# Performance work log

Hardware: AMD Instinct MI355X
Metric: run time of the kernel (lower is better)

The kernel has to match this reference:

```python
import math
import jax, jax.numpy as jnp
import numpy as np

D_MODEL = 1024
N_HEADS = 16
D_K = D_MODEL // N_HEADS


def _build_neighbours(n_heads):
    # Mirrors LatticeMultiHeadAttention._build_neighbours for a (4,4)-style lattice.
    side = int(math.sqrt(n_heads))
    cols = side + 1 if side * side < n_heads else side
    positions = [divmod(i, cols) for i in range(n_heads)]
    pos_map = {p: j for j, p in enumerate(positions)}
    nb_idx = np.full((n_heads, 8), -1, dtype=np.int64)
    nb_w = np.zeros((n_heads, 8), dtype=np.float32)
    for i, (r, c) in enumerate(positions):
        k = 0
        for dr in (-1, 0, 1):
            for dc in (-1, 0, 1):
                if dr == 0 and dc == 0:
                    continue
                j = pos_map.get((r + dr, c + dc))
                if j is not None and k < 8:
                    nb_idx[i, k] = j
                    nb_w[i, k] = math.exp(-math.hypot(dr, dc))
                    k += 1
    return nb_idx, nb_w


def _phase_biases(coupling):
    # Sequential Kuramoto phase update: head h uses neighbor phases already
    # updated for heads < h (exactly as the torch per-head loop mutates buffers).
    H = coupling.shape[0]
    nb_idx, nb_w = _build_neighbours(H)
    phases = [jnp.asarray(0.0, coupling.dtype) for _ in range(H)]
    two_pi = 2.0 * math.pi
    for h in range(H):
        force = jnp.asarray(0.0, coupling.dtype)
        for k in range(8):
            j = int(nb_idx[h, k])
            if j >= 0:
                force = force + jnp.asarray(nb_w[h, k], coupling.dtype) * jnp.sin(phases[j] - phases[h])
        intrinsic = 1.0 + 0.1 * h
        new_phase = (phases[h] + 0.01 * (intrinsic + coupling[h] * force)) % two_pi
        phases[h] = new_phase
    return 0.1 * jnp.cos(jnp.stack(phases))  # [H] per-head scalar bias


def setup_inputs() -> dict:
    key = jax.random.key(0)
    ks = jax.random.split(key, 9)
    B, L = 2, 2048
    std = 0.02
    return {
        "query": jax.random.normal(ks[0], (B, L, D_MODEL), jnp.float32),
        "key": jax.random.normal(ks[1], (B, L, D_MODEL), jnp.float32),
        "value": jax.random.normal(ks[2], (B, L, D_MODEL), jnp.float32),
        "Wq": std * jax.random.normal(ks[3], (N_HEADS, D_MODEL, D_K), jnp.float32),
        "Wk": std * jax.random.normal(ks[4], (N_HEADS, D_MODEL, D_K), jnp.float32),
        "Wv": std * jax.random.normal(ks[5], (N_HEADS, D_MODEL, D_K), jnp.float32),
        "out_w": std * jax.random.normal(ks[6], (D_MODEL, D_MODEL), jnp.float32),
        "out_b": jnp.zeros((D_MODEL,), jnp.float32),
        "coupling": 0.1 * jnp.ones((N_HEADS,), jnp.float32),
    }


def reference(query, key, value, Wq, Wk, Wv, out_w, out_b, coupling):
    d_k = Wq.shape[-1]
    Q = jnp.einsum("bld,hdk->bhlk", query, Wq)
    K = jnp.einsum("bld,hdk->bhlk", key, Wk)
    V = jnp.einsum("bld,hdk->bhlk", value, Wv)
    scale = jnp.asarray(math.sqrt(float(d_k)), query.dtype)
    scores = jnp.einsum("bhlk,bhmk->bhlm", Q, K) / scale
    bias = _phase_biases(coupling)  # [H]
    scores = scores + bias[None, :, None, None]
    attn = jax.nn.softmax(scores, axis=-1)
    ctx = jnp.einsum("bhlm,bhmk->bhlk", attn, V)
    B, H, L, _ = ctx.shape
    out = ctx.transpose(0, 2, 1, 3).reshape(B, L, H * d_k)  # concat heads
    return out @ out_w + out_b
```

## Files before the change

### kernel.cpp

```cpp
#include <hip/hip_runtime.h>
#include <cstdint>

typedef uint16_t u16;
typedef __attribute__((ext_vector_type(8))) short bf16x8;
typedef __attribute__((ext_vector_type(4))) short bf16x4;
typedef __attribute__((ext_vector_type(4))) float f32x4;

#define QSCALE 0.18033688011112042f

struct Ptr3 { const float* a; const float* b; const float* c; };

__device__ __forceinline__ u16 f2bf(float x) {
  union { float f; uint32_t u; } v; v.f = x;
  uint32_t r = (v.u + 0x7fffu + ((v.u >> 16) & 1u)) >> 16;
  return (u16)r;
}

#if __has_builtin(__builtin_amdgcn_cvt_pk_bf16_f32)
typedef __bf16 bf2_t __attribute__((ext_vector_type(2)));
__device__ __forceinline__ uint32_t pkbf(float a, float b) {
  bf2_t v = __builtin_amdgcn_cvt_pk_bf16_f32(a, b);
  uint32_t u;
  __builtin_memcpy(&u, &v, 4);
  return u;
}
#else
__device__ __forceinline__ uint32_t pkbf(float a, float b) {
  return (uint32_t)f2bf(a) | ((uint32_t)f2bf(b) << 16);
}
#endif

__device__ __forceinline__ void async16(void* lds, const void* g) {
  __builtin_amdgcn_global_load_lds((const __attribute__((address_space(1))) void*)g,
                                   (__attribute__((address_space(3))) void*)lds, 16, 0, 0);
}

__global__ __launch_bounds__(256) void k_prep(Ptr3 in, u16* __restrict__ out,
                                              Ptr3 w, const float* __restrict__ ow,
                                              u16* __restrict__ wt, u16* __restrict__ wto) {
  __shared__ u16 tile[64 * 65];
  const int t = threadIdx.x;
  const int bx = blockIdx.x;
  if (bx < 12288) {
    int z = bx >> 12;
    int i = (bx & 4095) * 256 + t;
    const float* p = z == 0 ? in.a : (z == 1 ? in.b : in.c);
    float4 v = ((const float4*)p)[i];
    uint2 o2;
    o2.x = pkbf(v.x, v.y);
    o2.y = pkbf(v.z, v.w);
    *(uint2*)(out + (long)z * 4194304 + (long)i * 4) = o2;
    return;
  }
  const int b2 = bx - 12288;
  const float* src;
  long in_base, out_base;
  int rstr, r0, c0;
  u16* outp;
  if (b2 < 768) {
    int z = b2 >> 4;
    r0 = (b2 & 15) * 64; c0 = 0;
    src = (z < 16) ? w.a : (z < 32 ? w.b : w.c);
    in_base = (long)(z & 15) * 65536;
    out_base = (long)z * 65536;
    rstr = 64; outp = wt;
  } else {
    int idx = b2 - 768;
    r0 = (idx >> 4) * 64; c0 = (idx & 15) * 64;
    src = ow; in_base = 0; out_base = 0;
    rstr = 1024; outp = wto;
  }
  for (int e = t; e < 4096; e += 256) {
    int rr = e >> 6, cc = e & 63;
    tile[rr * 65 + cc] = f2bf(src[in_base + (long)(r0 + rr) * rstr + c0 + cc]);
  }
  __syncthreads();
  for (int s = t; s < 512; s += 256) {
    int cc = s >> 3, r8 = (s & 7) << 3;
    bf16x8 p;
    #pragma unroll
    for (int j = 0; j < 8; ++j) p[j] = (short)tile[(r8 + j) * 65 + cc];
    *(bf16x8*)(outp + out_base + (long)(c0 + cc) * 1024 + r0 + r8) = p;
  }
}

__global__ __launch_bounds__(256) void k_gemm_qkv(const u16* __restrict__ A0,
                                                  const u16* __restrict__ B0,
                                                  u16* __restrict__ C0,
                                                  u16* __restrict__ Vt, float scale0) {
  __shared__ __align__(16) u16 smem[16640];
  u16* As = smem;
  u16* Bs = smem + 8192;
  u16* T  = smem;
  const int z = blockIdx.z;
  const u16* A = A0 + (long)z * 4194304;
  const u16* Bt = B0 + (long)z * 1048576;
  const int t = threadIdx.x, lane = t & 63, quad = lane >> 4, l16 = lane & 15;
  const int wave = t >> 6, wy = wave >> 1, wx = wave & 1;
  const int m0 = blockIdx.y * 128, n0 = blockIdx.x * 128;
  const int wbase = t & 192;
  f32x4 acc[4][4] = {};
  for (int k0 = 0; k0 < 1024; k0 += 64) {
    __syncthreads();
    #pragma unroll
    for (int i = 0; i < 4; ++i) {
      int sb = i * 256 + wbase;
      int s = sb + lane;
      int row = s >> 3, c = s & 7;
      int cs = c ^ (row & 7);
      async16(As + sb * 8, A + (long)(m0 + row) * 1024 + k0 + cs * 8);
      async16(Bs + sb * 8, Bt + (long)(n0 + row) * 1024 + k0 + cs * 8);
    }
    __syncthreads();
    #pragma unroll
    for (int kk = 0; kk < 2; ++kk) {
      bf16x8 af[4], bfr[4];
      #pragma unroll
      for (int mt = 0; mt < 4; ++mt) {
        int row = wy * 64 + mt * 16 + l16;
        int pos = (kk * 4 + quad) ^ (row & 7);
        af[mt] = *(const bf16x8*)(As + row * 64 + pos * 8);
      }
      #pragma unroll
      for (int nt = 0; nt < 4; ++nt) {
        int row = wx * 64 + nt * 16 + l16;
        int pos = (kk * 4 + quad) ^ (row & 7);
        bfr[nt] = *(const bf16x8*)(Bs + row * 64 + pos * 8);
      }
      #pragma unroll
      for (int mt = 0; mt < 4; ++mt)
        #pragma unroll
        for (int nt = 0; nt < 4; ++nt)
          acc[mt][nt] = __builtin_amdgcn_mfma_f32_16x16x32_bf16(af[mt], bfr[nt], acc[mt][nt], 0, 0, 0);
    }
  }
  if (z < 2) {
    u16* C = C0 + (long)z * 4194304;
    const float scale = z ? 1.0f : scale0;
    #pragma unroll
    for (int mt = 0; mt < 4; ++mt)
      #pragma unroll
      for (int nt = 0; nt < 4; ++nt) {
        int col = n0 + wx * 64 + nt * 16 + l16;
        int row = m0 + wy * 64 + mt * 16 + quad * 4;
        uint32_t ua = pkbf(acc[mt][nt][0] * scale, acc[mt][nt][1] * scale);
        uint32_t ub = pkbf(acc[mt][nt][2] * scale, acc[mt][nt][3] * scale);
        C[(long)row * 1024 + col] = (u16)ua;
        C[(long)(row + 1) * 1024 + col] = (u16)(ua >> 16);
        C[(long)(row + 2) * 1024 + col] = (u16)ub;
        C[(long)(row + 3) * 1024 + col] = (u16)(ub >> 16);
      }
  } else {
    __syncthreads();
    #pragma unroll
    for (int mt = 0; mt < 4; ++mt)
      #pragma unroll
      for (int nt = 0; nt < 4; ++nt) {
        int cc = wx * 64 + nt * 16 + l16;
        int rr = wy * 64 + mt * 16 + quad * 4;
        uint32_t ua = pkbf(acc[mt][nt][0], acc[mt][nt][1]);
        uint32_t ub = pkbf(acc[mt][nt][2], acc[mt][nt][3]);
        T[(rr + 0) * 130 + cc] = (u16)ua;
        T[(rr + 1) * 130 + cc] = (u16)(ua >> 16);
        T[(rr + 2) * 130 + cc] = (u16)ub;
        T[(rr + 3) * 130 + cc] = (u16)(ub >> 16);
      }
    __syncthreads();
    const int h0 = blockIdx.x * 2, bb = m0 >> 11, lb = m0 & 2047;
    #pragma unroll
    for (int i = 0; i < 8; ++i) {
      int s = t + i * 256;
      int c = s >> 4, l0 = (s & 15) * 8;
      bf16x8 p;
      #pragma unroll
      for (int j = 0; j < 8; ++j) p[j] = (short)T[(l0 + j) * 130 + c];
      *(bf16x8*)(Vt + (long)(bb * 16 + h0 + (c >> 6)) * 131072 +
                 (long)(c & 63) * 2048 + lb + l0) = p;
    }
  }
}

__global__ __launch_bounds__(256) void k_gemm_out(const u16* __restrict__ A,
                                                  const u16* __restrict__ Bt,
                                                  float* __restrict__ C,
                                                  const float* __restrict__ bias) {
  __shared__ __align__(16) u16 As[128 * 32];
  __shared__ __align__(16) u16 Bs[64 * 32];
  const int t = threadIdx.x, lane = t & 63, quad = lane >> 4, l16 = lane & 15;
  const int wave = t >> 6;
  const int m0 = blockIdx.y * 128, n0 = blockIdx.x * 64;
  const int wbase = t & 192;
  f32x4 acc[2][4] = {};
  for (int k0 = 0; k0 < 1024; k0 += 32) {
    __syncthreads();
    #pragma unroll
    for (int i = 0; i < 2; ++i) {
      int sb = i * 256 + wbase;
      int s = sb + lane;
      int row = s >> 2, c = s & 3;
      async16(As + sb * 8, A + (long)(m0 + row) * 1024 + k0 + c * 8);
    }
    {
      int s = t;
      int row = s >> 2, c = s & 3;
      async16(Bs + wbase * 8, Bt + (long)(n0 + row) * 1024 + k0 + c * 8);
    }
    __syncthreads();
    bf16x8 af[2], bfr[4];
    #pragma unroll
    for (int mt = 0; mt < 2; ++mt)
      af[mt] = *(const bf16x8*)(As + (wave * 32 + mt * 16 + l16) * 32 + quad * 8);
    #pragma unroll
    for (int nt = 0; nt < 4; ++nt)
      bfr[nt] = *(const bf16x8*)(Bs + (nt * 16 + l16) * 32 + quad * 8);
    #pragma unroll
    for (int mt = 0; mt < 2; ++mt)
      #pragma unroll
      for (int nt = 0; nt < 4; ++nt)
        acc[mt][nt] = __builtin_amdgcn_mfma_f32_16x16x32_bf16(af[mt], bfr[nt], acc[mt][nt], 0, 0, 0);
  }
  #pragma unroll
  for (int mt = 0; mt < 2; ++mt)
    #pragma unroll
    for (int nt = 0; nt < 4; ++nt) {
      int col = n0 + nt * 16 + l16;
      #pragma unroll
      for (int r = 0; r < 4; ++r) {
        int row = m0 + wave * 32 + mt * 16 + quad * 4 + r;
        C[(long)row * 1024 + col] = acc[mt][nt][r] + bias[col];
      }
    }
}

__global__ __launch_bounds__(512, 2) void k_flash(const u16* __restrict__ Qp,
                                                  const u16* __restrict__ Kp,
                                                  const u16* __restrict__ Vt,
                                                  u16* __restrict__ ctx) {
  __shared__ __align__(16) u16 qs[256 * 64];
  __shared__ __align__(16) u16 ks[64 * 72];
  __shared__ __align__(16) u16 vs[64 * 72];
  const int t = threadIdx.x, lane = t & 63, quad = lane >> 4, l16 = lane & 15;
  const int wave = t >> 6;
  const int bh = blockIdx.x & 31, b = bh >> 4, h = bh & 15;
  const int q0 = (blockIdx.x >> 5) * 256;
  const long gkbase = (long)b * 2097152 + h * 64;
  const long gvbase = (long)bh * 131072;
  const int srow = t >> 3, sc = t & 7;

  {
    long gq = (long)(b * 2048 + q0) * 1024 + h * 64;
    #pragma unroll
    for (int i = 0; i < 4; ++i) {
      int s = i * 512 + t;
      int row = s >> 3, pos = s & 7, c = pos ^ (row & 7);
      async16(qs + (long)s * 8, Qp + gq + (long)row * 1024 + c * 8);
    }
  }
  bf16x8 kreg = *(const bf16x8*)(Kp + gkbase + (long)srow * 1024 + sc * 8);
  bf16x8 vreg = *(const bf16x8*)(Vt + gvbase + (long)srow * 2048 + sc * 8);
  __syncthreads();

  bf16x8 qf[2][2];
  #pragma unroll
  for (int msub = 0; msub < 2; ++msub)
    #pragma unroll
    for (int kh = 0; kh < 2; ++kh) {
      int m = wave * 32 + msub * 16 + l16;
      int pos = (kh * 4 + quad) ^ (m & 7);
      qf[msub][kh] = *(const bf16x8*)(qs + m * 64 + pos * 8);
    }
  *(bf16x8*)(ks + srow * 72 + sc * 8) = kreg;
  *(bf16x8*)(vs + srow * 72 + sc * 8) = vreg;
  __syncthreads();

  u16* pw = qs + wave * 1152;

  float ls[2] = {};
  f32x4 o[2][4] = {};

  for (int kt = 0; kt < 32; ++kt) {
    if (kt < 31) {
      int kv0 = (kt + 1) * 64;
      kreg = *(const bf16x8*)(Kp + gkbase + (long)(kv0 + srow) * 1024 + sc * 8);
      vreg = *(const bf16x8*)(Vt + gvbase + kv0 + (long)srow * 2048 + sc * 8);
    }

    bf16x8 kf[4][2], vf[4][2];
    #pragma unroll
    for (int nt = 0; nt < 4; ++nt)
      #pragma unroll
      for (int kh = 0; kh < 2; ++kh) {
        kf[nt][kh] = *(const bf16x8*)(ks + (nt * 16 + l16) * 72 + kh * 32 + quad * 8);
        vf[nt][kh] = *(const bf16x8*)(vs + (nt * 16 + l16) * 72 + kh * 32 + quad * 8);
      }

    #pragma unroll
    for (int msub = 0; msub < 2; ++msub) {
      #pragma unroll
      for (int nt = 0; nt < 4; ++nt) {
        f32x4 a = {};
        #pragma unroll
        for (int kh = 0; kh < 2; ++kh)
          a = __builtin_amdgcn_mfma_f32_16x16x32_bf16(kf[nt][kh], qf[msub][kh], a, 0, 0, 0);
        float e0 = __builtin_amdgcn_exp2f(a[0]);
        float e1 = __builtin_amdgcn_exp2f(a[1]);
        float e2 = __builtin_amdgcn_exp2f(a[2]);
        float e3 = __builtin_amdgcn_exp2f(a[3]);
        ls[msub] += (e0 + e1) + (e2 + e3);
        uint2 w;
        w.x = pkbf(e0, e1);
        w.y = pkbf(e2, e3);
        *(uint2*)(pw + l16 * 72 + nt * 16 + quad * 4) = w;
      }
      #pragma unroll
      for (int kh = 0; kh < 2; ++kh) {
        bf16x8 pa = *(const bf16x8*)(pw + l16 * 72 + kh * 32 + quad * 8);
        #pragma unroll
        for (int nt = 0; nt < 4; ++nt)
          o[msub][nt] = __builtin_amdgcn_mfma_f32_16x16x32_bf16(pa, vf[nt][kh], o[msub][nt], 0, 0, 0);
      }
    }

    __syncthreads();
    if (kt < 31) {
      *(bf16x8*)(ks + srow * 72 + sc * 8) = kreg;
      *(bf16x8*)(vs + srow * 72 + sc * 8) = vreg;
    }
    __syncthreads();
  }

  #pragma unroll
  for (int msub = 0; msub < 2; ++msub) {
    float l = ls[msub];
    l += __shfl_xor(l, 16);
    l += __shfl_xor(l, 32);
    float linv = 1.0f / l;
    float li0 = __shfl(linv, quad * 4 + 0);
    float li1 = __shfl(linv, quad * 4 + 1);
    float li2 = __shfl(linv, quad * 4 + 2);
    float li3 = __shfl(linv, quad * 4 + 3);
    #pragma unroll
    for (int nt = 0; nt < 4; ++nt) {
      int q = q0 + wave * 32 + msub * 16 + quad * 4;
      long idx = (long)(b * 2048 + q) * 1024 + h * 64 + nt * 16 + l16;
      uint32_t ua = pkbf(o[msub][nt][0] * li0, o[msub][nt][1] * li1);
      uint32_t ub = pkbf(o[msub][nt][2] * li2, o[msub][nt][3] * li3);
      ctx[idx]        = (u16)ua;
      ctx[idx + 1024] = (u16)(ua >> 16);
      ctx[idx + 2048] = (u16)ub;
      ctx[idx + 3072] = (u16)(ub >> 16);
    }
  }
}

extern "C" void kernel_launch(void* const* d_in, const int* in_sizes, int n_in,
                              void* d_out, int out_size, void* d_ws, size_t ws_size,
                              hipStream_t stream) {
  const float* query = (const float*)d_in[0];
  const float* key   = (const float*)d_in[1];
  const float* value = (const float*)d_in[2];
  const float* Wq    = (const float*)d_in[3];
  const float* Wk    = (const float*)d_in[4];
  const float* Wv    = (const float*)d_in[5];
  const float* out_w = (const float*)d_in[6];
  const float* out_b = (const float*)d_in[7];
  float* out = (float*)d_out;

  char* ws = (char*)d_ws;
  size_t off = 0;
  auto alloc = [&](size_t bytes) {
    void* p = ws + off;
    off += (bytes + 255) & ~(size_t)255;
    return p;
  };
  u16* qb  = (u16*)alloc(4096L * 1024 * 2);
  u16* kb  = (u16*)alloc(4096L * 1024 * 2);
  u16* vb  = (u16*)alloc(4096L * 1024 * 2);
  u16* wtq = (u16*)alloc(1024L * 1024 * 2);
  u16* wtk = (u16*)alloc(1024L * 1024 * 2);
  u16* wtv = (u16*)alloc(1024L * 1024 * 2);
  u16* wto = (u16*)alloc(1024L * 1024 * 2);
  u16* Qp  = (u16*)alloc(4096L * 1024 * 2);
  u16* Kp  = (u16*)alloc(4096L * 1024 * 2);
  u16* Vtb = (u16*)alloc(4096L * 1024 * 2);
  u16* ctx = qb;
  (void)kb; (void)vb; (void)wtk; (void)wtv; (void)Kp;

  k_prep<<<13312, 256, 0, stream>>>(Ptr3{query, key, value}, qb,
                                    Ptr3{Wq, Wk, Wv}, out_w, wtq, wto);

  k_gemm_qkv<<<dim3(8, 32, 3), 256, 0, stream>>>(qb, wtq, Qp, Vtb, QSCALE);

  k_flash<<<256, 512, 0, stream>>>(Qp, Kp, Vtb, ctx);

  k_gemm_out<<<dim3(16, 32), 256, 0, stream>>>(ctx, wto, out, out_b);
}
```

Before: 231.2 us.

## Split KV tile across wave pairs with 64-row query groups and LDS merge

Each wave now owns 64 query rows and half of each 64-key tile, where it used to own 32 rows over the full tile. Wave pairs combine their partial outputs and row sums through LDS at the end. This cuts the K/V fragment loads from LDS per wave and widens the P-tile reuse across more query rows. In exchange it doubles the accumulator registers per wave, which risks lower occupancy under launch_bounds(512,2), and it adds a two-round LDS reduction epilogue.

Result: no change. 229.7 us (-0.6%).

```diff
diff --git a/kernel.cpp b/kernel.cpp
--- a/kernel.cpp
+++ b/kernel.cpp
@@ -236,11 +236,13 @@
                                                   const u16* __restrict__ Kp,
                                                   const u16* __restrict__ Vt,
                                                   u16* __restrict__ ctx) {
-  __shared__ __align__(16) u16 qs[256 * 64];
+  __shared__ __align__(16) u16 qs[16384];
   __shared__ __align__(16) u16 ks[64 * 72];
   __shared__ __align__(16) u16 vs[64 * 72];
+  __shared__ __align__(16) float lsb[1024];
   const int t = threadIdx.x, lane = t & 63, quad = lane >> 4, l16 = lane & 15;
   const int wave = t >> 6;
+  const int qg = wave >> 1, kvh = wave & 1;
   const int bh = blockIdx.x & 31, b = bh >> 4, h = bh & 15;
   const int q0 = (blockIdx.x >> 5) * 256;
   const long gkbase = (long)b * 2097152 + h * 64;
@@ -260,12 +262,12 @@
   bf16x8 vreg = *(const bf16x8*)(Vt + gvbase + (long)srow * 2048 + sc * 8);
   __syncthreads();
 
-  bf16x8 qf[2][2];
+  bf16x8 qf[4][2];
   #pragma unroll
-  for (int msub = 0; msub < 2; ++msub)
+  for (int msub = 0; msub < 4; ++msub)
     #pragma unroll
     for (int kh = 0; kh < 2; ++kh) {
-      int m = wave * 32 + msub * 16 + l16;
+      int m = qg * 64 + msub * 16 + l16;
       int pos = (kh * 4 + quad) ^ (m & 7);
       qf[msub][kh] = *(const bf16x8*)(qs + m * 64 + pos * 8);
     }
@@ -273,10 +275,11 @@
   *(bf16x8*)(vs + srow * 72 + sc * 8) = vreg;
   __syncthreads();
 
-  u16* pw = qs + wave * 1152;
-
-  float ls[2] = {};
-  f32x4 o[2][4] = {};
+  u16* pw = qs + wave * 2048;
+  const int pxor = l16 & 3;
+
+  float ls[4] = {};
+  f32x4 o[4][4] = {};
 
   for (int kt = 0; kt < 32; ++kt) {
     if (kt < 31) {
@@ -285,19 +288,20 @@
       vreg = *(const bf16x8*)(Vt + gvbase + kv0 + (long)srow * 2048 + sc * 8);
     }
 
-    bf16x8 kf[4][2], vf[4][2];
-    #pragma unroll
-    for (int nt = 0; nt < 4; ++nt)
-      #pragma unroll
-      for (int kh = 0; kh < 2; ++kh) {
-        kf[nt][kh] = *(const bf16x8*)(ks + (nt * 16 + l16) * 72 + kh * 32 + quad * 8);
-        vf[nt][kh] = *(const bf16x8*)(vs + (nt * 16 + l16) * 72 + kh * 32 + quad * 8);
-      }
-
-    #pragma unroll
-    for (int msub = 0; msub < 2; ++msub) {
-      #pragma unroll
-      for (int nt = 0; nt < 4; ++nt) {
+    bf16x8 kf[2][2], vf[4];
+    #pragma unroll
+    for (int nt = 0; nt < 2; ++nt)
+      #pragma unroll
+      for (int kh = 0; kh < 2; ++kh)
+        kf[nt][kh] = *(const bf16x8*)(ks + (kvh * 32 + nt * 16 + l16) * 72 + kh * 32 + quad * 8);
+    #pragma unroll
+    for (int dt = 0; dt < 4; ++dt)
+      vf[dt] = *(const bf16x8*)(vs + (dt * 16 + l16) * 72 + kvh * 32 + quad * 8);
+
+    #pragma unroll
+    for (int msub = 0; msub < 4; ++msub) {
+      #pragma unroll
+      for (int nt = 0; nt < 2; ++nt) {
         f32x4 a = {};
         #pragma unroll
         for (int kh = 0; kh < 2; ++kh)
@@ -310,15 +314,13 @@
         uint2 w;
         w.x = pkbf(e0, e1);
         w.y = pkbf(e2, e3);
-        *(uint2*)(pw + l16 * 72 + nt * 16 + quad * 4) = w;
-      }
-      #pragma unroll
-      for (int kh = 0; kh < 2; ++kh) {
-        bf16x8 pa = *(const bf16x8*)(pw + l16 * 72 + kh * 32 + quad * 8);
-        #pragma unroll
-        for (int nt = 0; nt < 4; ++nt)
-          o[msub][nt] = __builtin_amdgcn_mfma_f32_16x16x32_bf16(pa, vf[nt][kh], o[msub][nt], 0, 0, 0);
-      }
+        int cp = (nt * 2 + (quad >> 1)) ^ pxor;
+        *(uint2*)(pw + (msub * 16 + l16) * 32 + cp * 8 + (quad & 1) * 4) = w;
+      }
+      bf16x8 pa = *(const bf16x8*)(pw + (msub * 16 + l16) * 32 + (quad ^ pxor) * 8);
+      #pragma unroll
+      for (int dt = 0; dt < 4; ++dt)
+        o[msub][dt] = __builtin_amdgcn_mfma_f32_16x16x32_bf16(pa, vf[dt], o[msub][dt], 0, 0, 0);
     }
 
     __syncthreads();
@@ -330,25 +332,56 @@
   }
 
   #pragma unroll
-  for (int msub = 0; msub < 2; ++msub) {
-    float l = ls[msub];
-    l += __shfl_xor(l, 16);
-    l += __shfl_xor(l, 32);
-    float linv = 1.0f / l;
-    float li0 = __shfl(linv, quad * 4 + 0);
-    float li1 = __shfl(linv, quad * 4 + 1);
-    float li2 = __shfl(linv, quad * 4 + 2);
-    float li3 = __shfl(linv, quad * 4 + 3);
-    #pragma unroll
-    for (int nt = 0; nt < 4; ++nt) {
-      int q = q0 + wave * 32 + msub * 16 + quad * 4;
-      long idx = (long)(b * 2048 + q) * 1024 + h * 64 + nt * 16 + l16;
-      uint32_t ua = pkbf(o[msub][nt][0] * li0, o[msub][nt][1] * li1);
-      uint32_t ub = pkbf(o[msub][nt][2] * li2, o[msub][nt][3] * li3);
-      ctx[idx]        = (u16)ua;
-      ctx[idx + 1024] = (u16)(ua >> 16);
-      ctx[idx + 2048] = (u16)ub;
-      ctx[idx + 3072] = (u16)(ub >> 16);
+  for (int m = 0; m < 4; ++m) {
+    ls[m] += __shfl_xor(ls[m], 16);
+    ls[m] += __shfl_xor(ls[m], 32);
+  }
+  f32x4* mb = (f32x4*)qs;
+  f32x4* lb = (f32x4*)lsb;
+  for (int r = 0; r < 2; ++r) {
+    __syncthreads();
+    if ((wave & 1) && (qg >> 1) == r) {
+      f32x4* dst = mb + (qg & 1) * 1024 + lane;
+      #pragma unroll
+      for (int m = 0; m < 4; ++m)
+        #pragma unroll
+        for (int d = 0; d < 4; ++d)
+          dst[(m * 4 + d) * 64] = o[m][d];
+      f32x4 lp = {ls[0], ls[1], ls[2], ls[3]};
+      lb[qg * 64 + lane] = lp;
+    }
+    __syncthreads();
+    if (!(wave & 1) && (qg >> 1) == r) {
+      f32x4* src = mb + (qg & 1) * 1024 + lane;
+      #pragma unroll
+      for (int m = 0; m < 4; ++m)
+        #pragma unroll
+        for (int d = 0; d < 4; ++d)
+          o[m][d] += src[(m * 4 + d) * 64];
+      f32x4 lp = lb[qg * 64 + lane];
+      ls[0] += lp[0]; ls[1] += lp[1]; ls[2] += lp[2]; ls[3] += lp[3];
+    }
+  }
+
+  if (!(wave & 1)) {
+    #pragma unroll
+    for (int m = 0; m < 4; ++m) {
+      float linv = 1.0f / ls[m];
+      float li0 = __shfl(linv, quad * 4 + 0);
+      float li1 = __shfl(linv, quad * 4 + 1);
+      float li2 = __shfl(linv, quad * 4 + 2);
+      float li3 = __shfl(linv, quad * 4 + 3);
+      #pragma unroll
+      for (int dt = 0; dt < 4; ++dt) {
+        int q = q0 + qg * 64 + m * 16 + quad * 4;
+        long idx = (long)(b * 2048 + q) * 1024 + h * 64 + dt * 16 + l16;
+        uint32_t ua = pkbf(o[m][dt][0] * li0, o[m][dt][1] * li1);
+        uint32_t ub = pkbf(o[m][dt][2] * li2, o[m][dt][3] * li3);
+        ctx[idx]        = (u16)ua;
+        ctx[idx + 1024] = (u16)(ua >> 16);
+        ctx[idx + 2048] = (u16)ub;
+        ctx[idx + 3072] = (u16)(ub >> 16);
+      }
     }
   }
 }
```

## Enlarge output GEMM tiles with swizzled LDS and double-buffer flash K/V

Applied to the files above, without the earlier changes.

The output projection GEMM moves to 128x128 tiles with a 64-wide K step and an XOR-swizzled LDS layout, so each wave computes a 64x64 sub-tile and the A/B loads are reused more. The flash kernel loads Q fragments straight from global memory into registers instead of staging them through LDS. It also double-buffers the K/V shared tiles, which removes one barrier per iteration. The cost is more accumulator registers and fewer blocks for the GEMM, and extra LDS for the flash buffers, which may lower occupancy.

Result: no change. 235.0 us (+1.7%).

```diff
diff --git a/kernel.cpp b/kernel.cpp
--- a/kernel.cpp
+++ b/kernel.cpp
@@ -184,61 +184,70 @@
                                                   const u16* __restrict__ Bt,
                                                   float* __restrict__ C,
                                                   const float* __restrict__ bias) {
-  __shared__ __align__(16) u16 As[128 * 32];
-  __shared__ __align__(16) u16 Bs[64 * 32];
+  __shared__ __align__(16) u16 smem[16384];
+  u16* As = smem;
+  u16* Bs = smem + 8192;
   const int t = threadIdx.x, lane = t & 63, quad = lane >> 4, l16 = lane & 15;
-  const int wave = t >> 6;
-  const int m0 = blockIdx.y * 128, n0 = blockIdx.x * 64;
+  const int wave = t >> 6, wy = wave >> 1, wx = wave & 1;
+  const int m0 = blockIdx.y * 128, n0 = blockIdx.x * 128;
   const int wbase = t & 192;
-  f32x4 acc[2][4] = {};
-  for (int k0 = 0; k0 < 1024; k0 += 32) {
-    __syncthreads();
-    #pragma unroll
-    for (int i = 0; i < 2; ++i) {
+  f32x4 acc[4][4] = {};
+  for (int k0 = 0; k0 < 1024; k0 += 64) {
+    __syncthreads();
+    #pragma unroll
+    for (int i = 0; i < 4; ++i) {
       int sb = i * 256 + wbase;
       int s = sb + lane;
-      int row = s >> 2, c = s & 3;
-      async16(As + sb * 8, A + (long)(m0 + row) * 1024 + k0 + c * 8);
-    }
-    {
-      int s = t;
-      int row = s >> 2, c = s & 3;
-      async16(Bs + wbase * 8, Bt + (long)(n0 + row) * 1024 + k0 + c * 8);
-    }
-    __syncthreads();
-    bf16x8 af[2], bfr[4];
-    #pragma unroll
-    for (int mt = 0; mt < 2; ++mt)
-      af[mt] = *(const bf16x8*)(As + (wave * 32 + mt * 16 + l16) * 32 + quad * 8);
-    #pragma unroll
-    for (int nt = 0; nt < 4; ++nt)
-      bfr[nt] = *(const bf16x8*)(Bs + (nt * 16 + l16) * 32 + quad * 8);
-    #pragma unroll
-    for (int mt = 0; mt < 2; ++mt)
-      #pragma unroll
-      for (int nt = 0; nt < 4; ++nt)
-        acc[mt][nt] = __builtin_amdgcn_mfma_f32_16x16x32_bf16(af[mt], bfr[nt], acc[mt][nt], 0, 0, 0);
+      int row = s >> 3, c = s & 7;
+      int cs = c ^ (row & 7);
+      async16(As + sb * 8, A + (long)(m0 + row) * 1024 + k0 + cs * 8);
+      async16(Bs + sb * 8, Bt + (long)(n0 + row) * 1024 + k0 + cs * 8);
+    }
+    __syncthreads();
+    #pragma unroll
+    for (int kk = 0; kk < 2; ++kk) {
+      bf16x8 af[4], bfr[4];
+      #pragma unroll
+      for (int mt = 0; mt < 4; ++mt) {
+        int row = wy * 64 + mt * 16 + l16;
+        int pos = (kk * 4 + quad) ^ (row & 7);
+        af[mt] = *(const bf16x8*)(As + row * 64 + pos * 8);
+      }
+      #pragma unroll
+      for (int nt = 0; nt < 4; ++nt) {
+        int row = wx * 64 + nt * 16 + l16;
+        int pos = (kk * 4 + quad) ^ (row & 7);
+        bfr[nt] = *(const bf16x8*)(Bs + row * 64 + pos * 8);
+      }
+      #pragma unroll
+      for (int mt = 0; mt < 4; ++mt)
+        #pragma unroll
+        for (int nt = 0; nt < 4; ++nt)
+          acc[mt][nt] = __builtin_amdgcn_mfma_f32_16x16x32_bf16(af[mt], bfr[nt], acc[mt][nt], 0, 0, 0);
+    }
   }
   #pragma unroll
-  for (int mt = 0; mt < 2; ++mt)
-    #pragma unroll
-    for (int nt = 0; nt < 4; ++nt) {
-      int col = n0 + nt * 16 + l16;
-      #pragma unroll
-      for (int r = 0; r < 4; ++r) {
-        int row = m0 + wave * 32 + mt * 16 + quad * 4 + r;
-        C[(long)row * 1024 + col] = acc[mt][nt][r] + bias[col];
-      }
-    }
+  for (int nt = 0; nt < 4; ++nt) {
+    int col = n0 + wx * 64 + nt * 16 + l16;
+    float bv = bias[col];
+    #pragma unroll
+    for (int mt = 0; mt < 4; ++mt) {
+      int row = m0 + wy * 64 + mt * 16 + quad * 4;
+      C[(long)row * 1024 + col]       = acc[mt][nt][0] + bv;
+      C[(long)(row + 1) * 1024 + col] = acc[mt][nt][1] + bv;
+      C[(long)(row + 2) * 1024 + col] = acc[mt][nt][2] + bv;
+      C[(long)(row + 3) * 1024 + col] = acc[mt][nt][3] + bv;
+    }
+  }
 }
 
 __global__ __launch_bounds__(512, 2) void k_flash(const u16* __restrict__ Qp,
                                                   const u16* __restrict__ Kp,
                                                   const u16* __restrict__ Vt,
                                                   u16* __restrict__ ctx) {
-  __shared__ __align__(16) u16 qs[256 * 64];
-  __shared__ __align__(16) u16 ks[64 * 72];
-  __shared__ __align__(16) u16 vs[64 * 72];
+  __shared__ __align__(16) u16 ks[2][4608];
+  __shared__ __align__(16) u16 vs[2][4608];
+  __shared__ __align__(16) u16 ps[9216];
   const int t = threadIdx.x, lane = t & 63, quad = lane >> 4, l16 = lane & 15;
   const int wave = t >> 6;
   const int bh = blockIdx.x & 31, b = bh >> 4, h = bh & 15;
@@ -247,38 +256,36 @@
   const long gvbase = (long)bh * 131072;
   const int srow = t >> 3, sc = t & 7;
 
+  bf16x8 qf[2][2];
   {
     long gq = (long)(b * 2048 + q0) * 1024 + h * 64;
     #pragma unroll
-    for (int i = 0; i < 4; ++i) {
-      int s = i * 512 + t;
-      int row = s >> 3, pos = s & 7, c = pos ^ (row & 7);
-      async16(qs + (long)s * 8, Qp + gq + (long)row * 1024 + c * 8);
-    }
-  }
-  bf16x8 kreg = *(const bf16x8*)(Kp + gkbase + (long)srow * 1024 + sc * 8);
-  bf16x8 vreg = *(const bf16x8*)(Vt + gvbase + (long)srow * 2048 + sc * 8);
+    for (int msub = 0; msub < 2; ++msub)
+      #pragma unroll
+      for (int kh = 0; kh < 2; ++kh) {
+        int m = wave * 32 + msub * 16 + l16;
+        qf[msub][kh] = *(const bf16x8*)(Qp + gq + (long)m * 1024 + kh * 32 + quad * 8);
+      }
+  }
+  {
+    bf16x8 k0 = *(const bf16x8*)(Kp + gkbase + (long)srow * 1024 + sc * 8);
+    bf16x8 v0 = *(const bf16x8*)(Vt + gvbase + (long)srow * 2048 + sc * 8);
+    *(bf16x8*)(&ks[0][srow * 72 + sc * 8]) = k0;
+    *(bf16x8*)(&vs[0][srow * 72 + sc * 8]) = v0;
+  }
   __syncthreads();
 
-  bf16x8 qf[2][2];
-  #pragma unroll
-  for (int msub = 0; msub < 2; ++msub)
-    #pragma unroll
-    for (int kh = 0; kh < 2; ++kh) {
-      int m = wave * 32 + msub * 16 + l16;
-      int pos = (kh * 4 + quad) ^ (m & 7);
-      qf[msub][kh] = *(const bf16x8*)(qs + m * 64 + pos * 8);
-    }
-  *(bf16x8*)(ks + srow * 72 + sc * 8) = kreg;
-  *(bf16x8*)(vs + srow * 72 + sc * 8) = vreg;
-  __syncthreads();
-
-  u16* pw = qs + wave * 1152;
+  u16* pw = ps + wave * 1152;
 
   float ls[2] = {};
   f32x4 o[2][4] = {};
-
+  bf16x8 kreg, vreg;
+
+  #pragma unroll 2
   for (int kt = 0; kt < 32; ++kt) {
+    const u16* kc = ks[kt & 1];
+    const u16* vc = vs[kt & 1];
+
     if (kt < 31) {
       int kv0 = (kt + 1) * 64;
       kreg = *(const bf16x8*)(Kp + gkbase + (long)(kv0 + srow) * 1024 + sc * 8);
@@ -290,8 +297,8 @@
     for (int nt = 0; nt < 4; ++nt)
       #pragma unroll
       for (int kh = 0; kh < 2; ++kh) {
-        kf[nt][kh] = *(const bf16x8*)(ks + (nt * 16 + l16) * 72 + kh * 32 + quad * 8);
-        vf[nt][kh] = *(const bf16x8*)(vs + (nt * 16 + l16) * 72 + kh * 32 + quad * 8);
+        kf[nt][kh] = *(const bf16x8*)(kc + (nt * 16 + l16) * 72 + kh * 32 + quad * 8);
+        vf[nt][kh] = *(const bf16x8*)(vc + (nt * 16 + l16) * 72 + kh * 32 + quad * 8);
       }
 
     #pragma unroll
@@ -321,10 +328,11 @@
       }
     }
 
-    __syncthreads();
     if (kt < 31) {
-      *(bf16x8*)(ks + srow * 72 + sc * 8) = kreg;
-      *(bf16x8*)(vs + srow * 72 + sc * 8) = vreg;
+      u16* kn = ks[(kt + 1) & 1];
+      u16* vn = vs[(kt + 1) & 1];
+      *(bf16x8*)(&kn[srow * 72 + sc * 8]) = kreg;
+      *(bf16x8*)(&vn[srow * 72 + sc * 8]) = vreg;
     }
     __syncthreads();
   }
@@ -393,5 +401,5 @@
 
   k_flash<<<256, 512, 0, stream>>>(Qp, Kp, Vtb, ctx);
 
-  k_gemm_out<<<dim3(16, 32), 256, 0, stream>>>(ctx, wto, out, out_b);
-}
+  k_gemm_out<<<dim3(8, 32), 256, 0, stream>>>(ctx, wto, out, out_b);
+}
```

## Switch flash attention to 32x32x16 MFMA with register-resident P via permlane swap

Applied to the files above, without the earlier changes.

Rewrites the flash attention inner loop to use 32x32x16 bf16 MFMA tiles instead of 16x16x32, so each wave handles its 32 query rows in one tile. The exponentiated scores are repacked into the A-operand layout in registers with permlane32_swap (or a shuffle fallback), which removes the per-wave LDS write/read round trip for P. The row-sum reduction and output normalization are reworked for the new accumulator layout. This trades LDS traffic and instruction count for more accumulator registers and cross-lane permutes.

Result: faster. 223.5 us (-3.3%).

```diff
diff --git a/kernel.cpp b/kernel.cpp
--- a/kernel.cpp
+++ b/kernel.cpp
@@ -3,8 +3,8 @@
 
 typedef uint16_t u16;
 typedef __attribute__((ext_vector_type(8))) short bf16x8;
-typedef __attribute__((ext_vector_type(4))) short bf16x4;
 typedef __attribute__((ext_vector_type(4))) float f32x4;
+typedef __attribute__((ext_vector_type(16))) float f32x16;
 
 #define QSCALE 0.18033688011112042f
 
@@ -27,6 +27,23 @@
 #else
 __device__ __forceinline__ uint32_t pkbf(float a, float b) {
   return (uint32_t)f2bf(a) | ((uint32_t)f2bf(b) << 16);
+}
+#endif
+
+#if __has_builtin(__builtin_amdgcn_permlane32_swap)
+typedef __attribute__((ext_vector_type(2))) int i32x2;
+__device__ __forceinline__ void swap32(uint32_t& a, uint32_t& b, int hi) {
+  i32x2 r = __builtin_amdgcn_permlane32_swap((int)a, (int)b, false, false);
+  a = (uint32_t)r.x;
+  b = (uint32_t)r.y;
+}
+#else
+__device__ __forceinline__ void swap32(uint32_t& a, uint32_t& b, int hi) {
+  uint32_t ax = (uint32_t)__shfl_xor((int)a, 32);
+  uint32_t bx = (uint32_t)__shfl_xor((int)b, 32);
+  uint32_t na = hi ? bx : a;
+  uint32_t nb = hi ? b : ax;
+  a = na; b = nb;
 }
 #endif
 
@@ -239,7 +256,7 @@
   __shared__ __align__(16) u16 qs[256 * 64];
   __shared__ __align__(16) u16 ks[64 * 72];
   __shared__ __align__(16) u16 vs[64 * 72];
-  const int t = threadIdx.x, lane = t & 63, quad = lane >> 4, l16 = lane & 15;
+  const int t = threadIdx.x, lane = t & 63, hi = lane >> 5, l32 = lane & 31;
   const int wave = t >> 6;
   const int bh = blockIdx.x & 31, b = bh >> 4, h = bh & 15;
   const int q0 = (blockIdx.x >> 5) * 256;
@@ -260,23 +277,21 @@
   bf16x8 vreg = *(const bf16x8*)(Vt + gvbase + (long)srow * 2048 + sc * 8);
   __syncthreads();
 
-  bf16x8 qf[2][2];
-  #pragma unroll
-  for (int msub = 0; msub < 2; ++msub)
-    #pragma unroll
-    for (int kh = 0; kh < 2; ++kh) {
-      int m = wave * 32 + msub * 16 + l16;
-      int pos = (kh * 4 + quad) ^ (m & 7);
-      qf[msub][kh] = *(const bf16x8*)(qs + m * 64 + pos * 8);
-    }
+  bf16x8 qf[4];
+  {
+    int m = wave * 32 + l32;
+    #pragma unroll
+    for (int sd = 0; sd < 4; ++sd) {
+      int pos = (sd * 2 + hi) ^ (m & 7);
+      qf[sd] = *(const bf16x8*)(qs + m * 64 + pos * 8);
+    }
+  }
   *(bf16x8*)(ks + srow * 72 + sc * 8) = kreg;
   *(bf16x8*)(vs + srow * 72 + sc * 8) = vreg;
   __syncthreads();
 
-  u16* pw = qs + wave * 1152;
-
-  float ls[2] = {};
-  f32x4 o[2][4] = {};
+  float ls = 0.0f;
+  f32x16 o0 = {}, o1 = {};
 
   for (int kt = 0; kt < 32; ++kt) {
     if (kt < 31) {
@@ -285,40 +300,49 @@
       vreg = *(const bf16x8*)(Vt + gvbase + kv0 + (long)srow * 2048 + sc * 8);
     }
 
-    bf16x8 kf[4][2], vf[4][2];
-    #pragma unroll
-    for (int nt = 0; nt < 4; ++nt)
-      #pragma unroll
-      for (int kh = 0; kh < 2; ++kh) {
-        kf[nt][kh] = *(const bf16x8*)(ks + (nt * 16 + l16) * 72 + kh * 32 + quad * 8);
-        vf[nt][kh] = *(const bf16x8*)(vs + (nt * 16 + l16) * 72 + kh * 32 + quad * 8);
-      }
-
-    #pragma unroll
-    for (int msub = 0; msub < 2; ++msub) {
-      #pragma unroll
-      for (int nt = 0; nt < 4; ++nt) {
-        f32x4 a = {};
-        #pragma unroll
-        for (int kh = 0; kh < 2; ++kh)
-          a = __builtin_amdgcn_mfma_f32_16x16x32_bf16(kf[nt][kh], qf[msub][kh], a, 0, 0, 0);
-        float e0 = __builtin_amdgcn_exp2f(a[0]);
-        float e1 = __builtin_amdgcn_exp2f(a[1]);
-        float e2 = __builtin_amdgcn_exp2f(a[2]);
-        float e3 = __builtin_amdgcn_exp2f(a[3]);
-        ls[msub] += (e0 + e1) + (e2 + e3);
-        uint2 w;
-        w.x = pkbf(e0, e1);
-        w.y = pkbf(e2, e3);
-        *(uint2*)(pw + l16 * 72 + nt * 16 + quad * 4) = w;
-      }
-      #pragma unroll
-      for (int kh = 0; kh < 2; ++kh) {
-        bf16x8 pa = *(const bf16x8*)(pw + l16 * 72 + kh * 32 + quad * 8);
-        #pragma unroll
-        for (int nt = 0; nt < 4; ++nt)
-          o[msub][nt] = __builtin_amdgcn_mfma_f32_16x16x32_bf16(pa, vf[nt][kh], o[msub][nt], 0, 0, 0);
-      }
+    bf16x8 kf0[4], kf1[4], vf0[4], vf1[4];
+    #pragma unroll
+    for (int sd = 0; sd < 4; ++sd) {
+      kf0[sd] = *(const bf16x8*)(ks + (l32) * 72 + sd * 16 + hi * 8);
+      kf1[sd] = *(const bf16x8*)(ks + (32 + l32) * 72 + sd * 16 + hi * 8);
+      vf0[sd] = *(const bf16x8*)(vs + (l32) * 72 + sd * 16 + hi * 8);
+      vf1[sd] = *(const bf16x8*)(vs + (32 + l32) * 72 + sd * 16 + hi * 8);
+    }
+
+    f32x16 p0 = {}, p1 = {};
+    #pragma unroll
+    for (int sd = 0; sd < 4; ++sd) {
+      p0 = __builtin_amdgcn_mfma_f32_32x32x16_bf16(kf0[sd], qf[sd], p0, 0, 0, 0);
+      p1 = __builtin_amdgcn_mfma_f32_32x32x16_bf16(kf1[sd], qf[sd], p1, 0, 0, 0);
+    }
+    #pragma unroll
+    for (int r = 0; r < 16; ++r) {
+      float e0 = __builtin_amdgcn_exp2f(p0[r]);
+      float e1 = __builtin_amdgcn_exp2f(p1[r]);
+      p0[r] = e0; p1[r] = e1;
+      ls += e0 + e1;
+    }
+    #pragma unroll
+    for (int s = 0; s < 4; ++s) {
+      const int oct = (s & 1) * 8;
+      uint32_t xA, yA, xB, yB;
+      if (s < 2) {
+        xA = pkbf(p0[oct + 0], p0[oct + 1]);
+        yA = pkbf(p0[oct + 2], p0[oct + 3]);
+        xB = pkbf(p0[oct + 4], p0[oct + 5]);
+        yB = pkbf(p0[oct + 6], p0[oct + 7]);
+      } else {
+        xA = pkbf(p1[oct + 0], p1[oct + 1]);
+        yA = pkbf(p1[oct + 2], p1[oct + 3]);
+        xB = pkbf(p1[oct + 4], p1[oct + 5]);
+        yB = pkbf(p1[oct + 6], p1[oct + 7]);
+      }
+      swap32(xA, xB, hi);
+      swap32(yA, yB, hi);
+      union { uint32_t w[4]; bf16x8 v; } pa;
+      pa.w[0] = xA; pa.w[1] = yA; pa.w[2] = xB; pa.w[3] = yB;
+      o0 = __builtin_amdgcn_mfma_f32_32x32x16_bf16(pa.v, vf0[s], o0, 0, 0, 0);
+      o1 = __builtin_amdgcn_mfma_f32_32x32x16_bf16(pa.v, vf1[s], o1, 0, 0, 0);
     }
 
     __syncthreads();
@@ -329,27 +353,23 @@
     __syncthreads();
   }
 
+  ls += __shfl_xor(ls, 32);
+  float linv = 1.0f / ls;
+  float li[16];
   #pragma unroll
-  for (int msub = 0; msub < 2; ++msub) {
-    float l = ls[msub];
-    l += __shfl_xor(l, 16);
-    l += __shfl_xor(l, 32);
-    float linv = 1.0f / l;
-    float li0 = __shfl(linv, quad * 4 + 0);
-    float li1 = __shfl(linv, quad * 4 + 1);
-    float li2 = __shfl(linv, quad * 4 + 2);
-    float li3 = __shfl(linv, quad * 4 + 3);
-    #pragma unroll
-    for (int nt = 0; nt < 4; ++nt) {
-      int q = q0 + wave * 32 + msub * 16 + quad * 4;
-      long idx = (long)(b * 2048 + q) * 1024 + h * 64 + nt * 16 + l16;
-      uint32_t ua = pkbf(o[msub][nt][0] * li0, o[msub][nt][1] * li1);
-      uint32_t ub = pkbf(o[msub][nt][2] * li2, o[msub][nt][3] * li3);
-      ctx[idx]        = (u16)ua;
-      ctx[idx + 1024] = (u16)(ua >> 16);
-      ctx[idx + 2048] = (u16)ub;
-      ctx[idx + 3072] = (u16)(ub >> 16);
-    }
+  for (int r = 0; r < 16; ++r)
+    li[r] = __shfl(linv, (r & 3) + 8 * (r >> 2) + 4 * hi);
+
+  #pragma unroll
+  for (int r = 0; r < 16; r += 2) {
+    int q = q0 + wave * 32 + (r & 3) + 8 * (r >> 2) + 4 * hi;
+    long idx = (long)(b * 2048 + q) * 1024 + h * 64 + l32;
+    uint32_t u0 = pkbf(o0[r] * li[r], o0[r + 1] * li[r + 1]);
+    uint32_t u1 = pkbf(o1[r] * li[r], o1[r + 1] * li[r + 1]);
+    ctx[idx]             = (u16)u0;
+    ctx[idx + 1024]      = (u16)(u0 >> 16);
+    ctx[idx + 32]        = (u16)u1;
+    ctx[idx + 32 + 1024] = (u16)(u1 >> 16);
   }
 }
 
```
